# Kernel tuning notes

Measured on AMD Instinct MI355X. Metric: run time of the kernel, lower is better.

The kernel has to match this reference:

```python
import jax, jax.numpy as jnp
import numpy as np

D_STATE = 16
LOW_RANK = 6


def _scan_fwd(t):
    # 'interwave' scan: (B, stream, signal, C, H, W) -> (stream, B, C, H*W*signal)
    st, B, C = t.shape[1], t.shape[0], t.shape[3]
    t = jnp.transpose(t, (1, 0, 3, 4, 5, 2))  # stream,B,C,H,W,signal
    return t.reshape(st, B, C, -1)


def _scan_bwd(t, sg, H, W):
    # inverse 'interwave': (stream, B, C, H*W*sg) -> (B, stream, sg, C, H, W)
    st, B, C, _ = t.shape
    t = t.reshape(st, B, C, H, W, sg)
    return jnp.transpose(t, (1, 0, 5, 2, 3, 4))


def _layernorm(t, w, b):
    # LayerNorm over last (channel) axis, eps=1e-5 (torch default)
    mu = t.mean(-1, keepdims=True)
    var = t.var(-1, keepdims=True)
    return (t - mu) * jax.lax.rsqrt(var + 1e-5) * w + b


def reference(x, x_proj_weight, dt_projs_weight, dt_projs_bias, A_logs, Ds, norm_weight, norm_bias):
    B, S, C, H, W = x.shape
    stream = S + 1
    G = 4 * stream            # scan_direction * stream groups
    N = D_STATE
    R = LOW_RANK
    L = S * H * W             # unistream_length
    i = jnp.arange(S - 1)
    j = jnp.arange(S)

    # ---- CommDiffSS2DScan (cross-scan) ----
    x_comm_0 = _scan_fwd(x[:, None])                                  # (1,B,C,L)
    x_comm_1 = _scan_fwd(jnp.swapaxes(x, -1, -2)[:, None])
    x_dif = x[:, :, None] - x[:, None, :]                             # (B,S,S,C,H,W)
    x_dif = x_dif.at[:, i, i].set(x_dif[:, i, S - 1])
    x_dif = x_dif.at[:, :, S - 1].set(x)
    x_diff_0 = _scan_fwd(x_dif)                                       # (S,B,C,L)
    x_diff_1 = _scan_fwd(jnp.swapaxes(x_dif, -1, -2))
    xs0 = jnp.concatenate([x_diff_0, x_comm_0], 0)                    # (stream,B,C,L)
    xs1 = jnp.concatenate([x_diff_1, x_comm_1], 0)
    xs = jnp.stack([xs0, xs1, xs0[..., ::-1], xs1[..., ::-1]], 0)     # (4,stream,B,C,L)
    xs = jnp.transpose(xs, (2, 0, 1, 3, 4))                           # (B,4,stream,C,L)

    # ---- input-dependent projections ----
    x_dbl = jnp.einsum('bkscl,kspc->bkspl', xs, x_proj_weight)        # (B,4,stream,R+2N,L)
    dts, Bs, Cs = jnp.split(x_dbl, [R, R + N], axis=3)
    dts = jnp.einsum('bksrl,kscr->bkscl', dts, dt_projs_weight)       # (B,4,stream,C,L)

    u = xs.reshape(B, G, C, L)
    delta = jax.nn.softplus(dts.reshape(B, G, C, L) + dt_projs_bias.reshape(G, C)[None, :, :, None])
    A = -jnp.exp(A_logs).reshape(G, C, N)
    Bm = Bs.reshape(B, G, N, L)
    Cm = Cs.reshape(B, G, N, L)

    # ---- selective scan along L ----
    def step(h, inp):
        u_, d_, b_, c_ = inp                                          # (B,G,C),(B,G,C),(B,G,N),(B,G,N)
        h = h * jnp.exp(d_[..., None] * A) + (d_ * u_)[..., None] * b_[:, :, None, :]
        return h, jnp.einsum('bgcn,bgn->bgc', h, c_)

    h0 = jnp.zeros((B, G, C, N), x.dtype)
    _, ys = jax.lax.scan(step, h0, (jnp.moveaxis(u, -1, 0), jnp.moveaxis(delta, -1, 0),
                                    jnp.moveaxis(Bm, -1, 0), jnp.moveaxis(Cm, -1, 0)))
    ys = jnp.moveaxis(ys, 0, -1) + Ds.reshape(G, C)[None, :, :, None] * u  # (B,G,C,L)

    # ---- CommDiffSS2DMerge (cross-merge) ----
    ys = jnp.transpose(ys.reshape(B, 4, stream, C, L), (1, 2, 0, 3, 4))   # (4,stream,B,C,L)
    ys = ys[:2] + ys[2:, ..., ::-1]                                       # (2,stream,B,C,L)
    yd = _scan_bwd(ys[0, :S], S, H, W) + jnp.swapaxes(_scan_bwd(ys[1, :S], S, W, H), -1, -2)
    y = yd[:, :, S - 1]
    yd = yd.at[:, i, S - 1].set(yd[:, i, i])
    yd = yd.at[:, j, j].set(0.0)
    y_dif_extend = yd.sum(2)
    y_com = (_scan_bwd(ys[0, S:], S, H, W) + jnp.swapaxes(_scan_bwd(ys[1, S:], S, W, H), -1, -2)).reshape(B, S, C, H, W)

    tocl = lambda t: jnp.transpose(t, (0, 1, 3, 4, 2))  # channels-last for out_norm
    return (_layernorm(tocl(y), norm_weight, norm_bias),
            _layernorm(tocl(y_com), norm_weight, norm_bias),
            _layernorm(tocl(y_dif_extend), norm_weight, norm_bias))


def setup_inputs() -> dict:
    key = jax.random.key(0)
    ks = jax.random.split(key, 6)
    B, S, C, H, W = 4, 2, 96, 32, 32
    stream = S + 1
    G = 4 * stream
    N, R = D_STATE, LOW_RANK
    P = N + N + R
    return {
        'x': jax.random.normal(ks[0], (B, S, C, H, W), jnp.float32),
        'x_proj_weight': jax.random.normal(ks[1], (4, stream, P, C), jnp.float32) * 0.1,
        'dt_projs_weight': jax.random.normal(ks[2], (4, stream, C, R), jnp.float32) * 0.1,
        'dt_projs_bias': jax.random.uniform(ks[3], (G * C,), jnp.float32) * 0.1,
        'A_logs': jax.random.uniform(ks[4], (G * C, N), jnp.float32),
        'Ds': jax.random.normal(ks[5], (G * C,), jnp.float32) * 0.1,
        'norm_weight': jnp.ones((C,), jnp.float32),
        'norm_bias': jnp.zeros((C,), jnp.float32),
    }
```

## Files before the change

kernel.cpp:

```cpp
#include <hip/hip_runtime.h>
#include <math.h>

typedef float f4 __attribute__((ext_vector_type(4)));
typedef float f2 __attribute__((ext_vector_type(2)));

#define L_LEN 2048
#define C_DIM 96
#define N_DIM 16
#define R_DIM 6
#define G_DIM 12
#define B_DIM 4
#define NCHUNK 64
#define CLEN 32
#define BGC (B_DIM * G_DIM * C_DIM)

#define SZ_DELTA (B_DIM * G_DIM * L_LEN * C_DIM)
#define SZ_BC (B_DIM * G_DIM * N_DIM * L_LEN)
#define SZ_U6 (B_DIM * 6 * C_DIM * L_LEN)
#define SZ_Y (B_DIM * G_DIM * C_DIM * L_LEN)
#define SZ_H (BGC * NCHUNK * N_DIM)
#define SZ_S (BGC * NCHUNK)
#define SZ_X (B_DIM * 2 * C_DIM * 1024)
#define SZ_WPAD (G_DIM * 40 * C_DIM)

__device__ __forceinline__ float fexp2(float x) { return __builtin_amdgcn_exp2f(x); }

__device__ __forceinline__ float softplus_f(float x)
{
    float sp = __logf(1.f + __expf(x));
    return (x > 20.f) ? x : sp;
}

__global__ __launch_bounds__(256) void k0_xT(
    const float* __restrict__ x, float* __restrict__ xT)
{
    __shared__ float t[32][33];
    int img = blockIdx.x;
    const float* src = x + (size_t)img * 1024;
    float* dst = xT + (size_t)img * 1024;
    int tx = threadIdx.x & 31, ty = threadIdx.x >> 5;
#pragma unroll
    for (int r = 0; r < 32; r += 8) t[ty + r][tx] = src[(ty + r) * 32 + tx];
    __syncthreads();
#pragma unroll
    for (int r = 0; r < 32; r += 8) dst[(ty + r) * 32 + tx] = t[tx][ty + r];
}

__global__ __launch_bounds__(256) void k0b_padw(
    const float* __restrict__ xpw, float* __restrict__ wpad)
{
    int i = blockIdx.x * 256 + (int)threadIdx.x;
    if (i >= G_DIM * 40 * C_DIM) return;
    int g = i / (40 * C_DIM);
    int rem = i - g * 40 * C_DIM;
    int p = rem / C_DIM, c = rem - (rem / C_DIM) * C_DIM;
    wpad[i] = (p < 38) ? xpw[((size_t)g * 38 + p) * C_DIM + c] : 0.f;
}

__global__ __launch_bounds__(256) void k1_proj(
    const float* __restrict__ x, const float* __restrict__ xT,
    const float* __restrict__ wpad, const float* __restrict__ dtw,
    const float* __restrict__ dtb,
    float* __restrict__ deltaT, float* __restrict__ Bsw,
    float* __restrict__ Csw, float* __restrict__ u6T)
{
    __shared__ float Vsh[C_DIM * 68];
    __shared__ float Psh[40][65];

    int blk = blockIdx.x;
    int ltile = blk & 31;
    int bks = blk >> 5;
    int g = bks % G_DIM;
    int b = bks / G_DIM;
    const bool rev = (g >= 6);
    int gu = rev ? (g - 6) : g;
    int k = gu / 3, s = gu % 3;
    int l0 = ltile * 64;
    int bg = b * G_DIM + g;
    int tid = (int)threadIdx.x;

    const float* xb = (k ? xT : x) + (size_t)b * 2 * C_DIM * 1024;

#pragma unroll
    for (int j = 0; j < 6; ++j) {
        int e = tid + j * 256;
        int c = e >> 4;
        int llq = (e & 15) * 4;
        int pp = rev ? (1022 - ((l0 + llq) >> 1)) : ((l0 + llq) >> 1);
        f2 x0 = *(const f2*)(xb + (size_t)c * 1024 + pp);
        f2 x1 = *(const f2*)(xb + (size_t)(C_DIM + c) * 1024 + pp);
        f4 v;
        if (!rev) {
            if (s == 2)      { v[0] = x0.x; v[1] = x1.x; v[2] = x0.y; v[3] = x1.y; }
            else if (s == 1) { v[0] = x1.x - x0.x; v[1] = x1.x; v[2] = x1.y - x0.y; v[3] = x1.y; }
            else             { v[0] = x0.x - x1.x; v[1] = x0.x; v[2] = x0.y - x1.y; v[3] = x0.y; }
        } else {
            if (s == 2)      { v[0] = x1.y; v[1] = x0.y; v[2] = x1.x; v[3] = x0.x; }
            else if (s == 1) { v[0] = x1.y; v[1] = x1.y - x0.y; v[2] = x1.x; v[3] = x1.x - x0.x; }
            else             { v[0] = x0.y; v[1] = x0.y - x1.y; v[2] = x0.x; v[3] = x0.x - x1.x; }
        }
        *(f4*)(Vsh + c * 68 + llq) = v;
    }
    __syncthreads();

    if (!rev) {
        size_t ub = ((size_t)(b * 6 + g) * L_LEN + l0) * C_DIM;
#pragma unroll
        for (int j = 0; j < 6; ++j) {
            int e = tid + j * 256;
            int lidx = e / 24;
            int c4 = (e - lidx * 24) * 4;
            f4 v = { Vsh[(c4 + 0) * 68 + lidx], Vsh[(c4 + 1) * 68 + lidx],
                     Vsh[(c4 + 2) * 68 + lidx], Vsh[(c4 + 3) * 68 + lidx] };
            *(f4*)(u6T + ub + (size_t)lidx * C_DIM + c4) = v;
        }
    }

    int ll = tid & 63;
    int P0 = __builtin_amdgcn_readfirstlane((tid >> 6) * 10);
    const float* wp = wpad + (size_t)g * 3840 + (size_t)P0 * C_DIM;

    float acc[10];
#pragma unroll
    for (int p = 0; p < 10; ++p) acc[p] = 0.f;

    for (int cb = 0; cb < C_DIM; cb += 8) {
        float vc[8];
#pragma unroll
        for (int i = 0; i < 8; ++i) vc[i] = Vsh[(cb + i) * 68 + ll];
#pragma unroll
        for (int p = 0; p < 10; ++p) {
#pragma unroll
            for (int q = 0; q < 2; ++q) {
                f4 w = *(const f4*)(wp + p * C_DIM + cb + q * 4);
#pragma unroll
                for (int i = 0; i < 4; ++i)
                    acc[p] = fmaf(w[i], vc[q * 4 + i], acc[p]);
            }
        }
    }

    __syncthreads();
#pragma unroll
    for (int p = 0; p < 10; ++p) Psh[P0 + p][ll] = acc[p];
    __syncthreads();
    {
        int q = tid & 3, lx = tid >> 2;
        f4 bv = { Psh[6 + q * 4 + 0][lx], Psh[6 + q * 4 + 1][lx],
                  Psh[6 + q * 4 + 2][lx], Psh[6 + q * 4 + 3][lx] };
        *(f4*)(Bsw + ((size_t)bg * L_LEN + l0 + lx) * N_DIM + q * 4) = bv;
        f4 cv = { Psh[22 + q * 4 + 0][lx], Psh[22 + q * 4 + 1][lx],
                  Psh[22 + q * 4 + 2][lx], Psh[22 + q * 4 + 3][lx] };
        *(f4*)(Csw + ((size_t)bg * L_LEN + l0 + lx) * N_DIM + q * 4) = cv;
    }
    const float* wdg = dtw + (size_t)g * C_DIM * R_DIM;
    const float* biasg = dtb + g * C_DIM;
    size_t db = ((size_t)bg * L_LEN + l0) * C_DIM;
#pragma unroll
    for (int it = 0; it < 24; ++it) {
        int e = tid + it * 256;
        int lidx = e / 96, c = e - (e / 96) * 96;
        float dsum = biasg[c];
#pragma unroll
        for (int r = 0; r < R_DIM; ++r) dsum = fmaf(Psh[r][lidx], wdg[c * R_DIM + r], dsum);
        deltaT[db + (size_t)lidx * C_DIM + c] = softplus_f(dsum);
    }
}

__global__ __launch_bounds__(192) void k2_scanA(
    const float* __restrict__ deltaT, const float* __restrict__ Bsw,
    const float* __restrict__ u6T, const float* __restrict__ A_logs,
    float* __restrict__ hend, float* __restrict__ Sbuf)
{
    __shared__ f4 Bsh[256];
    int blk = blockIdx.x;
    int chgrp = blk & 31;
    int bg = blk >> 5;
    int g = bg % G_DIM;
    int b = bg / G_DIM;
    int tid = (int)threadIdx.x;

    const f4* Bg = (const f4*)(Bsw + ((size_t)bg * L_LEN + chgrp * 64) * N_DIM);
    for (int i = tid; i < 256; i += 192) Bsh[i] = Bg[i];
    __syncthreads();

    int chl = tid / 96;
    int c = tid % 96;
    int ch = chgrp * 2 + chl;
    int bgc = bg * C_DIM + c;
    const bool rev = (g >= 6);
    int gu = rev ? (g - 6) : g;

    float a2[N_DIM];
    {
        const f4* Ap = (const f4*)(A_logs + ((size_t)g * C_DIM + c) * N_DIM);
        f4 Av[4] = { Ap[0], Ap[1], Ap[2], Ap[3] };
#pragma unroll
        for (int n = 0; n < N_DIM; ++n)
            a2[n] = -__expf(Av[n >> 2][n & 3]) * 1.44269504f;
    }

    const int LOFF = ch * CLEN;
    const float* dp = deltaT + ((size_t)bg * L_LEN + LOFF) * C_DIM + c;
    const float* up;
    int us;
    if (rev) { up = u6T + ((size_t)(b * 6 + gu) * L_LEN + (2047 - LOFF)) * C_DIM + c; us = -C_DIM; }
    else     { up = u6T + ((size_t)(b * 6 + gu) * L_LEN + LOFF) * C_DIM + c; us = C_DIM; }

    float h[N_DIM];
#pragma unroll
    for (int n = 0; n < N_DIM; ++n) h[n] = 0.f;
    float S = 0.f;

    float dbuf[4], ubuf[4];
#pragma unroll
    for (int j = 0; j < 4; ++j) { dbuf[j] = dp[j * C_DIM]; ubuf[j] = up[j * us]; }

    for (int jj = 0; jj < CLEN; jj += 4) {
        int nx = (jj + 4 < CLEN) ? jj + 4 : jj;
        float dn[4], un[4];
#pragma unroll
        for (int j = 0; j < 4; ++j) { dn[j] = dp[(nx + j) * C_DIM]; un[j] = up[(nx + j) * us]; }
#pragma unroll
        for (int j = 0; j < 4; ++j) {
            int li = chl * CLEN + jj + j;
            float d = dbuf[j];
            S += d;
            float du = d * ubuf[j];
            const f4* Bl = Bsh + (size_t)li * 4;
            f4 Bv[4] = { Bl[0], Bl[1], Bl[2], Bl[3] };
#pragma unroll
            for (int n = 0; n < N_DIM; ++n) {
                float e = fexp2(d * a2[n]);
                h[n] = fmaf(h[n], e, du * Bv[n >> 2][n & 3]);
            }
        }
#pragma unroll
        for (int j = 0; j < 4; ++j) { dbuf[j] = dn[j]; ubuf[j] = un[j]; }
    }
    float* hp = hend + ((size_t)bgc * NCHUNK + ch) * N_DIM;
#pragma unroll
    for (int q = 0; q < 4; ++q) {
        f4 hv = { h[q * 4], h[q * 4 + 1], h[q * 4 + 2], h[q * 4 + 3] };
        *(f4*)(hp + q * 4) = hv;
    }
    Sbuf[(size_t)bgc * NCHUNK + ch] = S;
}

__global__ __launch_bounds__(256) void k2_fix(
    const float* __restrict__ Sbuf, const float* __restrict__ A_logs, float* hh)
{
    int t = blockIdx.x * 256 + (int)threadIdx.x;
    int n = t & 15;
    int bgc = t >> 4;
    int c = bgc % C_DIM;
    int g = (bgc / C_DIM) % G_DIM;
    float a2 = -__expf(A_logs[((size_t)g * C_DIM + c) * N_DIM + n]) * 1.44269504f;
    const float* Sp = Sbuf + (size_t)bgc * NCHUNK;
    float h = 0.f;
    for (int ch = 0; ch < NCHUNK; ++ch) {
        size_t idx = ((size_t)bgc * NCHUNK + ch) * N_DIM + n;
        float he = hh[idx];
        float P = fexp2(a2 * Sp[ch]);
        hh[idx] = h;
        h = fmaf(h, P, he);
    }
}

__global__ __launch_bounds__(192) void k2_scanC(
    const float* __restrict__ deltaT, const float* __restrict__ Bsw,
    const float* __restrict__ Csw, const float* __restrict__ u6T,
    const float* __restrict__ A_logs, const float* __restrict__ Ds,
    const float* __restrict__ hstart, float* __restrict__ yssT)
{
    __shared__ f4 Bsh[256];
    __shared__ f4 Csh[256];
    int blk = blockIdx.x;
    int chgrp = blk & 31;
    int bg = blk >> 5;
    int g = bg % G_DIM;
    int b = bg / G_DIM;
    int tid = (int)threadIdx.x;

    const f4* Bg = (const f4*)(Bsw + ((size_t)bg * L_LEN + chgrp * 64) * N_DIM);
    const f4* Cg = (const f4*)(Csw + ((size_t)bg * L_LEN + chgrp * 64) * N_DIM);
    for (int i = tid; i < 256; i += 192) { Bsh[i] = Bg[i]; Csh[i] = Cg[i]; }
    __syncthreads();

    int chl = tid / 96;
    int c = tid % 96;
    int ch = chgrp * 2 + chl;
    int bgc = bg * C_DIM + c;
    const bool rev = (g >= 6);
    int gu = rev ? (g - 6) : g;

    float a2[N_DIM];
    {
        const f4* Ap = (const f4*)(A_logs + ((size_t)g * C_DIM + c) * N_DIM);
        f4 Av[4] = { Ap[0], Ap[1], Ap[2], Ap[3] };
#pragma unroll
        for (int n = 0; n < N_DIM; ++n)
            a2[n] = -__expf(Av[n >> 2][n & 3]) * 1.44269504f;
    }
    float dsc = Ds[g * C_DIM + c];

    const int LOFF = ch * CLEN;
    const float* dp = deltaT + ((size_t)bg * L_LEN + LOFF) * C_DIM + c;
    const float* up;
    int us;
    if (rev) { up = u6T + ((size_t)(b * 6 + gu) * L_LEN + (2047 - LOFF)) * C_DIM + c; us = -C_DIM; }
    else     { up = u6T + ((size_t)(b * 6 + gu) * L_LEN + LOFF) * C_DIM + c; us = C_DIM; }
    float* yp = yssT + ((size_t)bg * L_LEN + LOFF) * C_DIM + c;

    float h[N_DIM];
    {
        const f4* Hp = (const f4*)(hstart + ((size_t)bgc * NCHUNK + ch) * N_DIM);
        f4 Hv[4] = { Hp[0], Hp[1], Hp[2], Hp[3] };
#pragma unroll
        for (int n = 0; n < N_DIM; ++n) h[n] = Hv[n >> 2][n & 3];
    }

    float dbuf[4], ubuf[4];
#pragma unroll
    for (int j = 0; j < 4; ++j) { dbuf[j] = dp[j * C_DIM]; ubuf[j] = up[j * us]; }

    for (int jj = 0; jj < CLEN; jj += 4) {
        int nx = (jj + 4 < CLEN) ? jj + 4 : jj;
        float dn[4], un[4];
#pragma unroll
        for (int j = 0; j < 4; ++j) { dn[j] = dp[(nx + j) * C_DIM]; un[j] = up[(nx + j) * us]; }
#pragma unroll
        for (int j = 0; j < 4; ++j) {
            int li = chl * CLEN + jj + j;
            float d = dbuf[j];
            float uu = ubuf[j];
            float du = d * uu;
            const f4* Bl = Bsh + (size_t)li * 4;
            const f4* Cl = Csh + (size_t)li * 4;
            f4 Bv[4] = { Bl[0], Bl[1], Bl[2], Bl[3] };
            f4 Cv[4] = { Cl[0], Cl[1], Cl[2], Cl[3] };
            float y0 = dsc * uu, y1 = 0.f, y2 = 0.f, y3 = 0.f;
#pragma unroll
            for (int q = 0; q < 4; ++q) {
                float e0 = fexp2(d * a2[q * 4 + 0]);
                float e1 = fexp2(d * a2[q * 4 + 1]);
                float e2 = fexp2(d * a2[q * 4 + 2]);
                float e3 = fexp2(d * a2[q * 4 + 3]);
                h[q * 4 + 0] = fmaf(h[q * 4 + 0], e0, du * Bv[q][0]);
                h[q * 4 + 1] = fmaf(h[q * 4 + 1], e1, du * Bv[q][1]);
                h[q * 4 + 2] = fmaf(h[q * 4 + 2], e2, du * Bv[q][2]);
                h[q * 4 + 3] = fmaf(h[q * 4 + 3], e3, du * Bv[q][3]);
                y0 = fmaf(h[q * 4 + 0], Cv[q][0], y0);
                y1 = fmaf(h[q * 4 + 1], Cv[q][1], y1);
                y2 = fmaf(h[q * 4 + 2], Cv[q][2], y2);
                y3 = fmaf(h[q * 4 + 3], Cv[q][3], y3);
            }
            yp[(jj + j) * C_DIM] = (y0 + y1) + (y2 + y3);
        }
#pragma unroll
        for (int j = 0; j < 4; ++j) { dbuf[j] = dn[j]; ubuf[j] = un[j]; }
    }
}

__global__ __launch_bounds__(256) void k3_out(
    const float* __restrict__ yssT, const float* __restrict__ nw,
    const float* __restrict__ nb, float* __restrict__ out)
{
    __shared__ float tA[32][97];
    __shared__ float tB[32][97];
    __shared__ float ps[4][8][32];
    __shared__ float stat[4][32];

    int blk = blockIdx.x;
    int h = blk & 31;
    int bs = blk >> 5;
    int so = bs & 1;
    int b = bs >> 1;
    int tid = (int)threadIdx.x;

    auto Y = [&](int g) { return yssT + (size_t)(b * 12 + g) * L_LEN * C_DIM; };
    const float* Y0 = Y(so);
    const float* Y0r = Y(6 + so);
    const float* Y1 = Y(3 + so);
    const float* Y1r = Y(9 + so);

#pragma unroll 2
    for (int it = 0; it < 24; ++it) {
        int idx = tid + it * 256;
        int c = idx % 96, rest = idx / 96;
        int w = rest >> 1, par = rest & 1;
        int a0 = h * 64 + rest;
        int a1 = w * 64 + 2 * h + par;
        float v = Y0[(size_t)a0 * C_DIM + c] + Y0r[(size_t)(2047 - a0) * C_DIM + c]
                + Y1[(size_t)a1 * C_DIM + c] + Y1r[(size_t)(2047 - a1) * C_DIM + c];
        if (par) tA[w][c] = v; else tB[w][c] = v;
    }
    __syncthreads();

    int w = tid & 31, cg = tid >> 5;
    float sA = 0, qA = 0, sB = 0, qB = 0;
#pragma unroll
    for (int j = 0; j < 12; ++j) {
        float yv = tA[w][cg * 12 + j], dv = tB[w][cg * 12 + j];
        sA += yv; qA += yv * yv; sB += dv; qB += dv * dv;
    }
    ps[0][cg][w] = sA; ps[1][cg][w] = qA; ps[2][cg][w] = sB; ps[3][cg][w] = qB;
    __syncthreads();
    if (tid < 32) {
        int ww = tid;
        float t0 = 0, t1 = 0, t2 = 0, t3 = 0;
#pragma unroll
        for (int q = 0; q < 8; ++q) {
            t0 += ps[0][q][ww]; t1 += ps[1][q][ww];
            t2 += ps[2][q][ww]; t3 += ps[3][q][ww];
        }
        float muA = t0 * (1.f / 96.f), eqA = t1 * (1.f / 96.f);
        float muB = t2 * (1.f / 96.f), eqB = t3 * (1.f / 96.f);
        stat[0][ww] = muA; stat[1][ww] = rsqrtf(eqA - muA * muA + 1e-5f);
        stat[2][ww] = muB; stat[3][ww] = rsqrtf(eqB - muB * muB + 1e-5f);
    }
    __syncthreads();
    size_t obase = (size_t)blk * 3072;
    for (int e = tid; e < 3072; e += 256) {
        int ww = e / 96, c = e % 96;
        float wc = nw[c], bc = nb[c];
        out[obase + e] = (tA[ww][c] - stat[0][ww]) * stat[1][ww] * wc + bc;
        out[2 * 786432 + obase + e] = (tB[ww][c] - stat[2][ww]) * stat[3][ww] * wc + bc;
    }
    __syncthreads();

    const float* Y2 = Y(2);
    const float* Y2r = Y(8);
    const float* Y3 = Y(5);
    const float* Y3r = Y(11);
#pragma unroll 2
    for (int it = 0; it < 12; ++it) {
        int idx = tid + it * 256;
        int c = idx % 96, w2 = idx / 96;
        int a0 = h * 64 + 2 * w2 + so;
        int a1 = w2 * 64 + 2 * h + so;
        float v = Y2[(size_t)a0 * C_DIM + c] + Y2r[(size_t)(2047 - a0) * C_DIM + c]
                + Y3[(size_t)a1 * C_DIM + c] + Y3r[(size_t)(2047 - a1) * C_DIM + c];
        tA[w2][c] = v;
    }
    __syncthreads();
    float sC = 0, qC = 0;
#pragma unroll
    for (int j = 0; j < 12; ++j) {
        float v = tA[w][cg * 12 + j];
        sC += v; qC += v * v;
    }
    ps[0][cg][w] = sC; ps[1][cg][w] = qC;
    __syncthreads();
    if (tid < 32) {
        int ww = tid;
        float t0 = 0, t1 = 0;
#pragma unroll
        for (int q = 0; q < 8; ++q) { t0 += ps[0][q][ww]; t1 += ps[1][q][ww]; }
        float mu = t0 * (1.f / 96.f), eq = t1 * (1.f / 96.f);
        stat[0][ww] = mu; stat[1][ww] = rsqrtf(eq - mu * mu + 1e-5f);
    }
    __syncthreads();
    for (int e = tid; e < 3072; e += 256) {
        int ww = e / 96, c = e % 96;
        out[786432 + obase + e] = (tA[ww][c] - stat[0][ww]) * stat[1][ww] * nw[c] + nb[c];
    }
}

extern "C" void kernel_launch(void* const* d_in, const int* in_sizes, int n_in,
                              void* d_out, int out_size, void* d_ws, size_t ws_size,
                              hipStream_t stream)
{
    const float* x = (const float*)d_in[0];
    const float* xpw = (const float*)d_in[1];
    const float* dtw = (const float*)d_in[2];
    const float* dtb = (const float*)d_in[3];
    const float* A_logs = (const float*)d_in[4];
    const float* Ds = (const float*)d_in[5];
    const float* nw = (const float*)d_in[6];
    const float* nb = (const float*)d_in[7];
    float* out = (float*)d_out;

    float* ws = (float*)d_ws;
    float* deltaT = ws;
    float* Bsw = deltaT + SZ_DELTA;
    float* Csw = Bsw + SZ_BC;
    float* u6T = Csw + SZ_BC;
    float* yssT = u6T + SZ_U6;
    float* xT = yssT;
    float* wpad = yssT + SZ_X;
    float* hend = yssT + SZ_Y;
    float* Sbuf = hend + SZ_H;

    k0_xT<<<dim3(768), dim3(256), 0, stream>>>(x, xT);
    k0b_padw<<<dim3(180), dim3(256), 0, stream>>>(xpw, wpad);
    k1_proj<<<dim3(48 * 32), dim3(256), 0, stream>>>(x, xT, wpad, dtw, dtb, deltaT, Bsw, Csw, u6T);
    k2_scanA<<<dim3(48 * 32), dim3(192), 0, stream>>>(deltaT, Bsw, u6T, A_logs, hend, Sbuf);
    k2_fix<<<dim3(288), dim3(256), 0, stream>>>(Sbuf, A_logs, hend);
    k2_scanC<<<dim3(48 * 32), dim3(192), 0, stream>>>(deltaT, Bsw, Csw, u6T, A_logs, Ds, hend, yssT);
    k3_out<<<dim3(256), dim3(256), 0, stream>>>(yssT, nw, nb, out);
}
```

Before: 133.2 us.

## Double projection tile length and use packed FMA for two positions per thread

The projection kernel now covers 128 sequence positions per block instead of 64, halving the grid. Each thread accumulates two adjacent positions with packed f2 FMAs, so every weight load is reused twice. Vsh and Psh now share one aliased shared-memory buffer to keep LDS usage in check. The cost is fewer blocks, which lowers occupancy and parallelism, and the larger per-thread register footprint.

Result: faster. 128.4 us (median of 2 runs) (-3.6%).

```diff
diff --git a/kernel.cpp b/kernel.cpp
--- a/kernel.cpp
+++ b/kernel.cpp
@@ -13,6 +13,7 @@
 #define NCHUNK 64
 #define CLEN 32
 #define BGC (B_DIM * G_DIM * C_DIM)
+#define VS 136
 
 #define SZ_DELTA (B_DIM * G_DIM * L_LEN * C_DIM)
 #define SZ_BC (B_DIM * G_DIM * N_DIM * L_LEN)
@@ -24,6 +25,7 @@
 #define SZ_WPAD (G_DIM * 40 * C_DIM)
 
 __device__ __forceinline__ float fexp2(float x) { return __builtin_amdgcn_exp2f(x); }
+__device__ __forceinline__ f2 pkfma(f2 a, f2 b, f2 c) { return __builtin_elementwise_fma(a, b, c); }
 
 __device__ __forceinline__ float softplus_f(float x)
 {
@@ -64,28 +66,29 @@
     float* __restrict__ deltaT, float* __restrict__ Bsw,
     float* __restrict__ Csw, float* __restrict__ u6T)
 {
-    __shared__ float Vsh[C_DIM * 68];
-    __shared__ float Psh[40][65];
+    __shared__ char smem[C_DIM * VS * 4];
+    float* Vsh = (float*)smem;
+    float (*Psh)[132] = (float(*)[132])smem;
 
     int blk = blockIdx.x;
-    int ltile = blk & 31;
-    int bks = blk >> 5;
+    int ltile = blk & 15;
+    int bks = blk >> 4;
     int g = bks % G_DIM;
     int b = bks / G_DIM;
     const bool rev = (g >= 6);
     int gu = rev ? (g - 6) : g;
     int k = gu / 3, s = gu % 3;
-    int l0 = ltile * 64;
+    int l0 = ltile * 128;
     int bg = b * G_DIM + g;
     int tid = (int)threadIdx.x;
 
     const float* xb = (k ? xT : x) + (size_t)b * 2 * C_DIM * 1024;
 
 #pragma unroll
-    for (int j = 0; j < 6; ++j) {
+    for (int j = 0; j < 12; ++j) {
         int e = tid + j * 256;
-        int c = e >> 4;
-        int llq = (e & 15) * 4;
+        int c = e >> 5;
+        int llq = (e & 31) * 4;
         int pp = rev ? (1022 - ((l0 + llq) >> 1)) : ((l0 + llq) >> 1);
         f2 x0 = *(const f2*)(xb + (size_t)c * 1024 + pp);
         f2 x1 = *(const f2*)(xb + (size_t)(C_DIM + c) * 1024 + pp);
@@ -99,19 +102,19 @@
             else if (s == 1) { v[0] = x1.y; v[1] = x1.y - x0.y; v[2] = x1.x; v[3] = x1.x - x0.x; }
             else             { v[0] = x0.y; v[1] = x0.y - x1.y; v[2] = x0.x; v[3] = x0.x - x1.x; }
         }
-        *(f4*)(Vsh + c * 68 + llq) = v;
+        *(f4*)(Vsh + c * VS + llq) = v;
     }
     __syncthreads();
 
     if (!rev) {
         size_t ub = ((size_t)(b * 6 + g) * L_LEN + l0) * C_DIM;
 #pragma unroll
-        for (int j = 0; j < 6; ++j) {
+        for (int j = 0; j < 12; ++j) {
             int e = tid + j * 256;
             int lidx = e / 24;
             int c4 = (e - lidx * 24) * 4;
-            f4 v = { Vsh[(c4 + 0) * 68 + lidx], Vsh[(c4 + 1) * 68 + lidx],
-                     Vsh[(c4 + 2) * 68 + lidx], Vsh[(c4 + 3) * 68 + lidx] };
+            f4 v = { Vsh[(c4 + 0) * VS + lidx], Vsh[(c4 + 1) * VS + lidx],
+                     Vsh[(c4 + 2) * VS + lidx], Vsh[(c4 + 3) * VS + lidx] };
             *(f4*)(u6T + ub + (size_t)lidx * C_DIM + c4) = v;
         }
     }
@@ -120,14 +123,15 @@
     int P0 = __builtin_amdgcn_readfirstlane((tid >> 6) * 10);
     const float* wp = wpad + (size_t)g * 3840 + (size_t)P0 * C_DIM;
 
-    float acc[10];
-#pragma unroll
-    for (int p = 0; p < 10; ++p) acc[p] = 0.f;
+    f2 acc2[10];
+#pragma unroll
+    for (int p = 0; p < 10; ++p) acc2[p] = (f2){0.f, 0.f};
 
     for (int cb = 0; cb < C_DIM; cb += 8) {
-        float vc[8];
-#pragma unroll
-        for (int i = 0; i < 8; ++i) vc[i] = Vsh[(cb + i) * 68 + ll];
+        f2 vc2[8];
+#pragma unroll
+        for (int i = 0; i < 8; ++i)
+            vc2[i] = *(const f2*)(Vsh + (cb + i) * VS + 2 * ll);
 #pragma unroll
         for (int p = 0; p < 10; ++p) {
 #pragma unroll
@@ -135,17 +139,21 @@
                 f4 w = *(const f4*)(wp + p * C_DIM + cb + q * 4);
 #pragma unroll
                 for (int i = 0; i < 4; ++i)
-                    acc[p] = fmaf(w[i], vc[q * 4 + i], acc[p]);
+                    acc2[p] = pkfma((f2){w[i], w[i]}, vc2[q * 4 + i], acc2[p]);
             }
         }
     }
 
     __syncthreads();
 #pragma unroll
-    for (int p = 0; p < 10; ++p) Psh[P0 + p][ll] = acc[p];
-    __syncthreads();
-    {
-        int q = tid & 3, lx = tid >> 2;
+    for (int p = 0; p < 10; ++p) {
+        Psh[P0 + p][2 * ll] = acc2[p].x;
+        Psh[P0 + p][2 * ll + 1] = acc2[p].y;
+    }
+    __syncthreads();
+#pragma unroll
+    for (int half = 0; half < 2; ++half) {
+        int q = tid & 3, lx = (tid >> 2) + half * 64;
         f4 bv = { Psh[6 + q * 4 + 0][lx], Psh[6 + q * 4 + 1][lx],
                   Psh[6 + q * 4 + 2][lx], Psh[6 + q * 4 + 3][lx] };
         *(f4*)(Bsw + ((size_t)bg * L_LEN + l0 + lx) * N_DIM + q * 4) = bv;
@@ -159,11 +167,16 @@
 #pragma unroll
     for (int it = 0; it < 24; ++it) {
         int e = tid + it * 256;
-        int lidx = e / 96, c = e - (e / 96) * 96;
-        float dsum = biasg[c];
-#pragma unroll
-        for (int r = 0; r < R_DIM; ++r) dsum = fmaf(Psh[r][lidx], wdg[c * R_DIM + r], dsum);
-        deltaT[db + (size_t)lidx * C_DIM + c] = softplus_f(dsum);
+        int lp = e / 96, c = e - (e / 96) * 96;
+        const float* wrow = wdg + c * R_DIM;
+        f2 ds2 = { biasg[c], biasg[c] };
+#pragma unroll
+        for (int r = 0; r < R_DIM; ++r) {
+            f2 pv = { Psh[r][2 * lp], Psh[r][2 * lp + 1] };
+            ds2 = pkfma((f2){wrow[r], wrow[r]}, pv, ds2);
+        }
+        deltaT[db + (size_t)(2 * lp) * C_DIM + c] = softplus_f(ds2.x);
+        deltaT[db + (size_t)(2 * lp + 1) * C_DIM + c] = softplus_f(ds2.y);
     }
 }
 
@@ -494,7 +507,7 @@
 
     k0_xT<<<dim3(768), dim3(256), 0, stream>>>(x, xT);
     k0b_padw<<<dim3(180), dim3(256), 0, stream>>>(xpw, wpad);
-    k1_proj<<<dim3(48 * 32), dim3(256), 0, stream>>>(x, xT, wpad, dtw, dtb, deltaT, Bsw, Csw, u6T);
+    k1_proj<<<dim3(48 * 16), dim3(256), 0, stream>>>(x, xT, wpad, dtw, dtb, deltaT, Bsw, Csw, u6T);
     k2_scanA<<<dim3(48 * 32), dim3(192), 0, stream>>>(deltaT, Bsw, u6T, A_logs, hend, Sbuf);
     k2_fix<<<dim3(288), dim3(256), 0, stream>>>(Sbuf, A_logs, hend);
     k2_scanC<<<dim3(48 * 32), dim3(192), 0, stream>>>(deltaT, Bsw, Csw, u6T, A_logs, Ds, hend, yssT);
```
